# Kernel tuning notes

Hardware: AMD Instinct MI355X
Metric: run time of the kernel (lower is better)

## Reference

```python
import jax, jax.numpy as jnp
import numpy as np

N_NODES = 50000
N_EDGES = 800000
IN_DIM = 256
HIDDEN = 32
HEADS = 4
OUT_DIM = 64


def setup_inputs() -> dict:
    key = jax.random.key(0)
    k1, k2, k3, k4, k5, k6, k7 = jax.random.split(key, 7)
    h = jax.random.normal(k1, (N_NODES, IN_DIM), dtype=jnp.float32)
    src = jax.random.randint(k2, (N_EDGES,), 0, N_NODES, dtype=jnp.int32)
    dst = jax.random.randint(k3, (N_EDGES,), 0, N_NODES, dtype=jnp.int32)
    # xavier_normal with relu gain, per-head weights
    gain = float(np.sqrt(2.0))
    W1 = gain * jnp.sqrt(2.0 / (IN_DIM + HIDDEN)) * jax.random.normal(k4, (HEADS, IN_DIM, HIDDEN), dtype=jnp.float32)
    a1 = gain * jnp.sqrt(2.0 / (2 * HIDDEN + 1)) * jax.random.normal(k5, (HEADS, 2 * HIDDEN), dtype=jnp.float32)
    W2 = gain * jnp.sqrt(2.0 / (HIDDEN * HEADS + OUT_DIM)) * jax.random.normal(k6, (1, HIDDEN * HEADS, OUT_DIM), dtype=jnp.float32)
    a2 = gain * jnp.sqrt(2.0 / (2 * OUT_DIM + 1)) * jax.random.normal(k7, (1, 2 * OUT_DIM), dtype=jnp.float32)
    return {"h": h, "src": src, "dst": dst, "W1": W1, "a1": a1, "W2": W2, "a2": a2}


def _gat_layer(x, src, dst, W, a):
    # x: [N, in], W: [H, in, d], a: [H, 2d]
    N = x.shape[0]
    d = W.shape[-1]
    z = jnp.einsum('ni,hio->nho', x, W)                    # [N, H, d]
    a_s, a_d = a[:, :d], a[:, d:]
    es = jnp.einsum('nho,ho->nh', z, a_s)                  # per-node src score
    ed = jnp.einsum('nho,ho->nh', z, a_d)                  # per-node dst score
    e = jax.nn.leaky_relu(es[src] + ed[dst])               # [E, H]
    # segment (per-destination) softmax over incoming edges
    emax = jax.ops.segment_max(e, dst, num_segments=N)     # [N, H]
    ex = jnp.exp(e - emax[dst])
    denom = jax.ops.segment_sum(ex, dst, num_segments=N)   # [N, H]
    alpha = ex / denom[dst]                                # [E, H]
    # scatter weighted sum of source feats back to destinations
    out = jax.ops.segment_sum(alpha[:, :, None] * z[src], dst, num_segments=N)  # [N, H, d]
    return out.reshape(N, -1)


def reference(h, src, dst, W1, a1, W2, a2):
    h1 = jax.nn.elu(_gat_layer(h, src, dst, W1, a1))       # [N, HEADS*HIDDEN]
    return _gat_layer(h1, src, dst, W2, a2)                # [N, OUT_DIM]
```

## Files before the change

### kernel.cpp

```cpp
#include <hip/hip_runtime.h>
#include <hip/hip_bf16.h>
#include <math.h>

#define N_NODES 50000
#define N_EDGES 800000
#define IN_DIM 256
#define HID 32
#define HEADS 4
#define OUT_DIM 64

#define SCAN_CHUNK 1024
#define SCAN_BLOCKS ((N_NODES + SCAN_CHUNK - 1) / SCAN_CHUNK)

typedef __attribute__((ext_vector_type(8))) short bf16x8;
typedef __attribute__((ext_vector_type(4))) float f32x4;

__device__ __forceinline__ float lrelu(float e) { return e > 0.f ? e : 0.01f * e; }
__device__ __forceinline__ float bflo(unsigned u) { return __uint_as_float(u << 16); }
__device__ __forceinline__ float bfhi(unsigned u) { return __uint_as_float(u & 0xffff0000u); }

__device__ __forceinline__ unsigned short rne_bf16(float x) {
    unsigned u = __float_as_uint(x);
    unsigned r = u + 0x7fffu + ((u >> 16) & 1u);
    return (unsigned short)(r >> 16);
}

__device__ __forceinline__ void splitf(float x, short& hi, short& lo) {
    unsigned u = __float_as_uint(x);
    unsigned short h = (unsigned short)(u >> 16);
    float hf = __uint_as_float(((unsigned)h) << 16);
    float l = x - hf;
    unsigned short lb = (unsigned short)(__float_as_uint(l) >> 16);
    hi = (short)h;
    lo = (short)lb;
}


__global__ void __launch_bounds__(256) prep_kernel(
        const float* __restrict__ W1, const float* __restrict__ a1,
        const float* __restrict__ W2, const float* __restrict__ a2,
        unsigned short* __restrict__ B1h, unsigned short* __restrict__ B1l,
        unsigned short* __restrict__ B2h, unsigned short* __restrict__ B2l,
        int* __restrict__ count) {
    int gid = blockIdx.x * 256 + threadIdx.x;
    if (gid < N_NODES) count[gid] = 0;

    int k = blockIdx.x;
    int c = threadIdx.x;
    if (c < 144) {
        float val = 0.f;
        if (c < 128) {
            val = W1[(size_t)(c >> 5) * IN_DIM * HID + (size_t)k * HID + (c & 31)];
        } else if (c < 136) {
            int j = c - 128;
            int hd = (j < 4) ? j : (j - 4);
            int off = (j < 4) ? 0 : HID;
            const float* Wp = W1 + (size_t)hd * IN_DIM * HID + (size_t)k * HID;
            const float* ap = a1 + hd * 2 * HID + off;
            float s = 0.f;
            for (int o = 0; o < HID; o++) s += Wp[o] * ap[o];
            val = s;
        }
        unsigned short hi = rne_bf16(val);
        float hf = __uint_as_float(((unsigned)hi) << 16);
        unsigned short lo = rne_bf16(val - hf);
        int s_ = k >> 5, q = (k >> 3) & 3, j8 = k & 7;
        int nt = c >> 4, L = q * 16 + (c & 15);
        size_t idx = (((size_t)s_ * 9 + nt) * 64 + L) * 8 + j8;
        B1h[idx] = hi;
        B1l[idx] = lo;
    } else if (c >= 160 && c < 240 && k < 128) {
        int c2 = c - 160;
        float val = 0.f;
        if (c2 < 64) {
            val = W2[(size_t)k * OUT_DIM + c2];
        } else if (c2 < 66) {
            const float* ap = a2 + (c2 - 64) * OUT_DIM;
            const float* Wp = W2 + (size_t)k * OUT_DIM;
            float s = 0.f;
            for (int o = 0; o < OUT_DIM; o++) s += Wp[o] * ap[o];
            val = s;
        }
        unsigned short hi = rne_bf16(val);
        float hf = __uint_as_float(((unsigned)hi) << 16);
        unsigned short lo = rne_bf16(val - hf);
        int s_ = k >> 5, q = (k >> 3) & 3, j8 = k & 7;
        int nt = c2 >> 4, L = q * 16 + (c2 & 15);
        size_t idx = (((size_t)s_ * 5 + nt) * 64 + L) * 8 + j8;
        B2h[idx] = hi;
        B2l[idx] = lo;
    }
}


__global__ void hist_kernel(const int* __restrict__ dst, int* __restrict__ count,
                            int* __restrict__ rank) {
    int i = blockIdx.x * blockDim.x + threadIdx.x;
    if (i < N_EDGES) rank[i] = atomicAdd(&count[dst[i]], 1);
}

__global__ void scan1_kernel(const int* __restrict__ count, int* __restrict__ row_start,
                             int* __restrict__ blocksum) {
    __shared__ int sdata[256];
    int t = threadIdx.x;
    int base = blockIdx.x * SCAN_CHUNK + t * 4;
    int v[4];
    int s = 0;
#pragma unroll
    for (int j = 0; j < 4; j++) {
        int idx = base + j;
        int x = (idx < N_NODES) ? count[idx] : 0;
        v[j] = x;
        s += x;
    }
    sdata[t] = s;
    __syncthreads();
    for (int off = 1; off < 256; off <<= 1) {
        int u = (t >= off) ? sdata[t - off] : 0;
        __syncthreads();
        sdata[t] += u;
        __syncthreads();
    }
    int excl = sdata[t] - s;
#pragma unroll
    for (int j = 0; j < 4; j++) {
        int idx = base + j;
        if (idx < N_NODES) row_start[idx] = excl;
        excl += v[j];
    }
    if (t == 255) blocksum[blockIdx.x] = sdata[255];
}

__global__ void scan23_kernel(int* __restrict__ row_start, const int* __restrict__ blocksum) {
    __shared__ int pre;
    int t = threadIdx.x;
    if (t < 64) {
        int v = (t < SCAN_BLOCKS) ? blocksum[t] : 0;
#pragma unroll
        for (int off = 1; off < 64; off <<= 1) {
            int u = __shfl_up(v, off);
            if (t >= off) v += u;
        }
        if (t == blockIdx.x) pre = v - blocksum[t];
    }
    __syncthreads();
    int add = pre;
    int base = blockIdx.x * SCAN_CHUNK + t * 4;
#pragma unroll
    for (int j = 0; j < 4; j++) {
        int idx = base + j;
        if (idx < N_NODES) row_start[idx] += add;
    }
}

__global__ void scatter_kernel(const int* __restrict__ src, const int* __restrict__ dst,
                               const int* __restrict__ rank, const int* __restrict__ row_start,
                               int* __restrict__ esrc) {
    int i = blockIdx.x * blockDim.x + threadIdx.x;
    if (i < N_EDGES) esrc[row_start[dst[i]] + rank[i]] = src[i];
}


__global__ void __launch_bounds__(256) proj1_mfma(
        const float* __restrict__ h, const unsigned short* __restrict__ Bh,
        const unsigned short* __restrict__ Bl, __hip_bfloat16* __restrict__ z1b,
        float* __restrict__ es1, float* __restrict__ ed1) {
    int tid = threadIdx.x;
    int wave = tid >> 6;
    int L = tid & 63;
    int q = L >> 4, L15 = L & 15;
    int n0 = blockIdx.x * 64 + wave * 16;

    int rowA = n0 + L15;
    int rrA = rowA < N_NODES ? rowA : N_NODES - 1;
    const float* hrow = h + (size_t)rrA * IN_DIM + q * 8;

    f32x4 acc[9];
#pragma unroll
    for (int nt = 0; nt < 9; nt++) acc[nt] = (f32x4)(0.f);

    float4 x0 = *(const float4*)(hrow);
    float4 x1 = *(const float4*)(hrow + 4);

#pragma unroll
    for (int s = 0; s < 8; s++) {
        int sn = (s < 7) ? s + 1 : 7;
        float4 p0 = *(const float4*)(hrow + sn * 32);
        float4 p1 = *(const float4*)(hrow + sn * 32 + 4);

        float xs[8] = {x0.x, x0.y, x0.z, x0.w, x1.x, x1.y, x1.z, x1.w};
        bf16x8 ah, al;
#pragma unroll
        for (int j = 0; j < 8; j++) {
            short hi, lo;
            splitf(xs[j], hi, lo);
            ah[j] = hi;
            al[j] = lo;
        }

        const bf16x8* bhp = (const bf16x8*)(Bh + ((size_t)s * 9 * 64) * 8 + (size_t)L * 8);
        const bf16x8* blp = (const bf16x8*)(Bl + ((size_t)s * 9 * 64) * 8 + (size_t)L * 8);
#pragma unroll
        for (int nt = 0; nt < 9; nt++) {
            bf16x8 bh = bhp[nt * 64];
            acc[nt] = __builtin_amdgcn_mfma_f32_16x16x32_bf16(ah, bh, acc[nt], 0, 0, 0);
            acc[nt] = __builtin_amdgcn_mfma_f32_16x16x32_bf16(al, bh, acc[nt], 0, 0, 0);
        }
        {
            bf16x8 bl8 = blp[8 * 64];
            acc[8] = __builtin_amdgcn_mfma_f32_16x16x32_bf16(ah, bl8, acc[8], 0, 0, 0);
        }
        x0 = p0;
        x1 = p1;
    }

#pragma unroll
    for (int r = 0; r < 4; r++) {
        int rowc = n0 + q * 4 + r;
        if (rowc < N_NODES) {
#pragma unroll
            for (int nt = 0; nt < 8; nt++)
                z1b[(size_t)rowc * 128 + nt * 16 + L15] = __float2bfloat16(acc[nt][r]);
            if (L15 < 4) es1[rowc * HEADS + L15] = acc[8][r];
            else if (L15 < 8) ed1[rowc * HEADS + (L15 - 4)] = acc[8][r];
        }
    }
}


__global__ void __launch_bounds__(256) proj2_mfma(
        const float* __restrict__ h1, const unsigned short* __restrict__ Bh,
        const unsigned short* __restrict__ Bl, __hip_bfloat16* __restrict__ z2b,
        float* __restrict__ es2, float* __restrict__ ed2) {
    int tid = threadIdx.x;
    int wave = tid >> 6;
    int L = tid & 63;
    int q = L >> 4, L15 = L & 15;
    int n0 = blockIdx.x * 64 + wave * 16;

    int rowA = n0 + L15;
    int rrA = rowA < N_NODES ? rowA : N_NODES - 1;
    const float* hrow = h1 + (size_t)rrA * 128 + q * 8;

    f32x4 acc[5];
#pragma unroll
    for (int nt = 0; nt < 5; nt++) acc[nt] = (f32x4)(0.f);

    float4 x0 = *(const float4*)(hrow);
    float4 x1 = *(const float4*)(hrow + 4);

#pragma unroll
    for (int s = 0; s < 4; s++) {
        int sn = (s < 3) ? s + 1 : 3;
        float4 p0 = *(const float4*)(hrow + sn * 32);
        float4 p1 = *(const float4*)(hrow + sn * 32 + 4);

        float xs[8] = {x0.x, x0.y, x0.z, x0.w, x1.x, x1.y, x1.z, x1.w};
        bf16x8 ah, al;
#pragma unroll
        for (int j = 0; j < 8; j++) {
            short hi, lo;
            splitf(xs[j], hi, lo);
            ah[j] = hi;
            al[j] = lo;
        }

        const bf16x8* bhp = (const bf16x8*)(Bh + ((size_t)s * 5 * 64) * 8 + (size_t)L * 8);
        const bf16x8* blp = (const bf16x8*)(Bl + ((size_t)s * 5 * 64) * 8 + (size_t)L * 8);
#pragma unroll
        for (int nt = 0; nt < 5; nt++) {
            bf16x8 bh = bhp[nt * 64];
            acc[nt] = __builtin_amdgcn_mfma_f32_16x16x32_bf16(ah, bh, acc[nt], 0, 0, 0);
            acc[nt] = __builtin_amdgcn_mfma_f32_16x16x32_bf16(al, bh, acc[nt], 0, 0, 0);
        }
        {
            bf16x8 bl4 = blp[4 * 64];
            acc[4] = __builtin_amdgcn_mfma_f32_16x16x32_bf16(ah, bl4, acc[4], 0, 0, 0);
        }
        x0 = p0;
        x1 = p1;
    }

#pragma unroll
    for (int r = 0; r < 4; r++) {
        int rowc = n0 + q * 4 + r;
        if (rowc < N_NODES) {
#pragma unroll
            for (int nt = 0; nt < 4; nt++)
                z2b[(size_t)rowc * OUT_DIM + nt * 16 + L15] = __float2bfloat16(acc[nt][r]);
            if (L15 == 0) es2[rowc] = acc[4][r];
            else if (L15 == 1) ed2[rowc] = acc[4][r];
        }
    }
}


__global__ void __launch_bounds__(256) agg1_kernel(
        const __hip_bfloat16* __restrict__ z1b, const float* __restrict__ es1,
        const float* __restrict__ ed1, const int* __restrict__ row_start,
        const int* __restrict__ count, const int* __restrict__ esrc,
        float* __restrict__ h1) {
    int v = blockIdx.x * 4 + (threadIdx.x >> 6);
    int L = threadIdx.x & 63;
    int half = L >> 5;
    int lj = L & 31;
    int sub = L >> 4;
    int c16 = L & 15;
    int hd = c16 >> 2;
    int srcl = (hd >> 1) << 5;
    int par = hd & 1;
    int beg = row_start[v], deg = count[v];
    float2 edp = *(const float2*)(ed1 + v * 4 + 2 * half);
    float lx = 0.f, ly = 0.f;
    float acc[8];
#pragma unroll
    for (int i = 0; i < 8; i++) acc[i] = 0.f;
    const uint4* zq = (const uint4*)z1b;

    for (int j0 = 0; j0 < deg; j0 += 32) {
        int chunk = min(32, deg - j0);
        bool valid = (j0 + lj) < deg;
        int s_o = 0;
        if (L < 32 && valid) s_o = esrc[beg + j0 + L];
        int s_e = __shfl(s_o, lj);
        float px = 0.f, py = 0.f;
        if (valid) {
            float2 es = *(const float2*)(es1 + (size_t)s_e * 4 + 2 * half);
            px = __expf(lrelu(es.x + edp.x));
            py = __expf(lrelu(es.y + edp.y));
        }
        lx += px;
        ly += py;

        int iters = (chunk + 15) & ~15;
        for (int j = 0; j < iters; j += 16) {
            int se[4];
            float qv[4];
            uint4 u[4];
#pragma unroll
            for (int g = 0; g < 4; g++) {
                int e = j + g * 4 + sub;
                se[g] = __shfl(s_o, e);
                float pxv = __shfl(px, srcl | e);
                float pyv = __shfl(py, srcl | e);
                qv[g] = par ? pyv : pxv;
                u[g] = zq[(size_t)se[g] * 16 + c16];
            }
#pragma unroll
            for (int g = 0; g < 4; g++) {
                acc[0] = fmaf(qv[g], bflo(u[g].x), acc[0]);
                acc[1] = fmaf(qv[g], bfhi(u[g].x), acc[1]);
                acc[2] = fmaf(qv[g], bflo(u[g].y), acc[2]);
                acc[3] = fmaf(qv[g], bfhi(u[g].y), acc[3]);
                acc[4] = fmaf(qv[g], bflo(u[g].z), acc[4]);
                acc[5] = fmaf(qv[g], bfhi(u[g].z), acc[5]);
                acc[6] = fmaf(qv[g], bflo(u[g].w), acc[6]);
                acc[7] = fmaf(qv[g], bfhi(u[g].w), acc[7]);
            }
        }
    }
#pragma unroll
    for (int off = 16; off >= 1; off >>= 1) {
        lx += __shfl_xor(lx, off);
        ly += __shfl_xor(ly, off);
    }
#pragma unroll
    for (int i = 0; i < 8; i++) {
        acc[i] += __shfl_xor(acc[i], 16);
        acc[i] += __shfl_xor(acc[i], 32);
    }
    float lxv = __shfl(lx, srcl);
    float lyv = __shfl(ly, srcl);
    float lmine = par ? lyv : lxv;
    if (L < 16) {
        float4 r0, r1;
#pragma unroll
        for (int i = 0; i < 8; i++) {
            float r = (deg > 0) ? acc[i] / lmine : 0.f;
            r = r > 0.f ? r : expm1f(r);
            if (i < 4) (&r0.x)[i] = r;
            else (&r1.x)[i - 4] = r;
        }
        float* dst = h1 + (size_t)v * 128 + c16 * 8;
        *(float4*)dst = r0;
        *(float4*)(dst + 4) = r1;
    }
}


__global__ void __launch_bounds__(256) agg2_kernel(
        const __hip_bfloat16* __restrict__ z2b, const float* __restrict__ es2,
        const float* __restrict__ ed2, const int* __restrict__ row_start,
        const int* __restrict__ count, const int* __restrict__ esrc,
        float* __restrict__ out) {
    int v = blockIdx.x * 4 + (threadIdx.x >> 6);
    int L = threadIdx.x & 63;
    int sub = L >> 3;
    int c8 = L & 7;
    int beg = row_start[v], deg = count[v];
    float edv = ed2[v];
    float l = 0.f;
    float acc[8];
#pragma unroll
    for (int i = 0; i < 8; i++) acc[i] = 0.f;
    const uint4* zq = (const uint4*)z2b;

    for (int j0 = 0; j0 < deg; j0 += 64) {
        int chunk = min(64, deg - j0);
        int s_o = 0;
        float p_o = 0.f;
        if (j0 + L < deg) {
            s_o = esrc[beg + j0 + L];
            p_o = __expf(lrelu(es2[s_o] + edv));
        }
        l += p_o;

        int iters = (chunk + 15) & ~15;
        for (int j = 0; j < iters; j += 16) {
            int se[2];
            float qv[2];
            uint4 u[2];
#pragma unroll
            for (int g = 0; g < 2; g++) {
                int e = j + g * 8 + sub;
                se[g] = __shfl(s_o, e);
                qv[g] = __shfl(p_o, e);
                u[g] = zq[(size_t)se[g] * 8 + c8];
            }
#pragma unroll
            for (int g = 0; g < 2; g++) {
                acc[0] = fmaf(qv[g], bflo(u[g].x), acc[0]);
                acc[1] = fmaf(qv[g], bfhi(u[g].x), acc[1]);
                acc[2] = fmaf(qv[g], bflo(u[g].y), acc[2]);
                acc[3] = fmaf(qv[g], bfhi(u[g].y), acc[3]);
                acc[4] = fmaf(qv[g], bflo(u[g].z), acc[4]);
                acc[5] = fmaf(qv[g], bfhi(u[g].z), acc[5]);
                acc[6] = fmaf(qv[g], bflo(u[g].w), acc[6]);
                acc[7] = fmaf(qv[g], bfhi(u[g].w), acc[7]);
            }
        }
    }
#pragma unroll
    for (int off = 32; off >= 1; off >>= 1)
        l += __shfl_xor(l, off);
#pragma unroll
    for (int i = 0; i < 8; i++) {
        acc[i] += __shfl_xor(acc[i], 8);
        acc[i] += __shfl_xor(acc[i], 16);
        acc[i] += __shfl_xor(acc[i], 32);
    }
    if (L < 8) {
        float4 r0, r1;
#pragma unroll
        for (int i = 0; i < 8; i++) {
            float r = (deg > 0) ? acc[i] / l : 0.f;
            if (i < 4) (&r0.x)[i] = r;
            else (&r1.x)[i - 4] = r;
        }
        float* dst = out + (size_t)v * OUT_DIM + c8 * 8;
        *(float4*)dst = r0;
        *(float4*)(dst + 4) = r1;
    }
}


extern "C" void kernel_launch(void* const* d_in, const int* in_sizes, int n_in,
                              void* d_out, int out_size, void* d_ws, size_t ws_size,
                              hipStream_t stream) {
    const float* h  = (const float*)d_in[0];
    const int* src  = (const int*)d_in[1];
    const int* dst  = (const int*)d_in[2];
    const float* W1 = (const float*)d_in[3];
    const float* a1 = (const float*)d_in[4];
    const float* W2 = (const float*)d_in[5];
    const float* a2 = (const float*)d_in[6];
    float* out = (float*)d_out;

    char* w = (char*)d_ws;
    size_t off = 0;
    auto alloc = [&](size_t bytes) {
        void* p = w + off;
        off = (off + bytes + 255) & ~(size_t)255;
        return p;
    };
    __hip_bfloat16* z1b = (__hip_bfloat16*)alloc((size_t)N_NODES * 128 * 2);
    float* es1 = (float*)alloc((size_t)N_NODES * HEADS * 4);
    float* ed1 = (float*)alloc((size_t)N_NODES * HEADS * 4);
    float* h1  = (float*)alloc((size_t)N_NODES * 128 * 4);
    __hip_bfloat16* z2b = (__hip_bfloat16*)alloc((size_t)N_NODES * OUT_DIM * 2);
    float* es2 = (float*)alloc((size_t)N_NODES * 4);
    float* ed2 = (float*)alloc((size_t)N_NODES * 4);
    int* count     = (int*)alloc((size_t)N_NODES * 4);
    int* row_start = (int*)alloc((size_t)N_NODES * 4);
    int* rank      = (int*)alloc((size_t)N_EDGES * 4);
    int* blocksum  = (int*)alloc((size_t)SCAN_BLOCKS * 4);
    int* esrc      = (int*)alloc((size_t)N_EDGES * 4);
    unsigned short* Bf1h = (unsigned short*)alloc((size_t)8 * 9 * 64 * 8 * 2);
    unsigned short* Bf1l = (unsigned short*)alloc((size_t)8 * 9 * 64 * 8 * 2);
    unsigned short* Bf2h = (unsigned short*)alloc((size_t)4 * 5 * 64 * 8 * 2);
    unsigned short* Bf2l = (unsigned short*)alloc((size_t)4 * 5 * 64 * 8 * 2);

    prep_kernel<<<256, 256, 0, stream>>>(W1, a1, W2, a2, Bf1h, Bf1l, Bf2h, Bf2l, count);
    hist_kernel<<<(N_EDGES + 255) / 256, 256, 0, stream>>>(dst, count, rank);
    scan1_kernel<<<SCAN_BLOCKS, 256, 0, stream>>>(count, row_start, blocksum);
    scan23_kernel<<<SCAN_BLOCKS, 256, 0, stream>>>(row_start, blocksum);
    scatter_kernel<<<(N_EDGES + 255) / 256, 256, 0, stream>>>(src, dst, rank, row_start, esrc);

    const int MBLK = (N_NODES + 63) / 64;
    proj1_mfma<<<MBLK, 256, 0, stream>>>(h, Bf1h, Bf1l, z1b, es1, ed1);
    agg1_kernel<<<N_NODES / 4, 256, 0, stream>>>(z1b, es1, ed1, row_start, count, esrc, h1);
    proj2_mfma<<<MBLK, 256, 0, stream>>>(h1, Bf2h, Bf2l, z2b, es2, ed2);
    agg2_kernel<<<N_NODES / 4, 256, 0, stream>>>(z2b, es2, ed2, row_start, count, esrc, out);
}
```

Measured before the change: 251.1 us.

## Precompute edge softmax weights in separate kernels and store h1 as bf16

Adds edge1_p and edge2_p kernels that compute exp(leaky_relu) attention numerators per edge in CSR order, so the aggregation kernels no longer gather es scores and compute exps inline. The aggregation loops are restructured to batch 8 (or 4) edge loads before the feature gathers, which exposes more memory-level parallelism. Layer-1 output h1 is now written as bf16 after ELU, and proj2 consumes it directly with a single MFMA pass instead of the hi/lo split. This halves the h1 traffic and MFMA count at the cost of precision, and adds two extra launches plus p1/p2/edst buffers.

```diff
diff --git a/kernel.cpp b/kernel.cpp
--- a/kernel.cpp
+++ b/kernel.cpp
@@ -155,9 +155,14 @@
 
 __global__ void scatter_kernel(const int* __restrict__ src, const int* __restrict__ dst,
                                const int* __restrict__ rank, const int* __restrict__ row_start,
-                               int* __restrict__ esrc) {
+                               int* __restrict__ esrc, int* __restrict__ edst) {
     int i = blockIdx.x * blockDim.x + threadIdx.x;
-    if (i < N_EDGES) esrc[row_start[dst[i]] + rank[i]] = src[i];
+    if (i < N_EDGES) {
+        int d = dst[i];
+        int pos = row_start[d] + rank[i];
+        esrc[pos] = src[i];
+        edst[pos] = d;
+    }
 }
 
 
@@ -228,8 +233,109 @@
 }
 
 
+__global__ void edge1_p(const int* __restrict__ esrc, const int* __restrict__ edst,
+                        const float* __restrict__ es1, const float* __restrict__ ed1,
+                        float* __restrict__ p1) {
+    int pos = blockIdx.x * 256 + threadIdx.x;
+    if (pos >= N_EDGES) return;
+    int s = esrc[pos], d = edst[pos];
+    float4 es = *(const float4*)(es1 + 4 * (size_t)s);
+    float4 ed = *(const float4*)(ed1 + 4 * (size_t)d);
+    p1[0 * (size_t)N_EDGES + pos] = __expf(lrelu(es.x + ed.x));
+    p1[1 * (size_t)N_EDGES + pos] = __expf(lrelu(es.y + ed.y));
+    p1[2 * (size_t)N_EDGES + pos] = __expf(lrelu(es.z + ed.z));
+    p1[3 * (size_t)N_EDGES + pos] = __expf(lrelu(es.w + ed.w));
+}
+
+__global__ void edge2_p(const int* __restrict__ esrc, const int* __restrict__ edst,
+                        const float* __restrict__ es2, const float* __restrict__ ed2,
+                        float* __restrict__ p2) {
+    int pos = blockIdx.x * 256 + threadIdx.x;
+    if (pos >= N_EDGES) return;
+    p2[pos] = __expf(lrelu(es2[esrc[pos]] + ed2[edst[pos]]));
+}
+
+
+__global__ void __launch_bounds__(256) agg1_kernel(
+        const __hip_bfloat16* __restrict__ z1b, const float* __restrict__ p1,
+        const int* __restrict__ row_start, const int* __restrict__ count,
+        const int* __restrict__ esrc, __hip_bfloat16* __restrict__ h1b) {
+    int v = blockIdx.x * 4 + (threadIdx.x >> 6);
+    int L = threadIdx.x & 63;
+    int sub = L >> 4;
+    int c16 = L & 15;
+    int hd = c16 >> 2;
+    int beg = row_start[v], deg = count[v];
+    const float* ph = p1 + (size_t)hd * N_EDGES + beg;
+    const int* ep = esrc + beg;
+    float lacc = 0.f;
+    float acc[8];
+#pragma unroll
+    for (int i = 0; i < 8; i++) acc[i] = 0.f;
+    const uint4* zq = (const uint4*)z1b;
+
+    for (int j0 = 0; j0 < deg; j0 += 32) {
+        int se[8];
+        float q[8];
+        uint4 u[8];
+#pragma unroll
+        for (int g = 0; g < 8; g++) {
+            if (j0 + g * 4 < deg) {
+                int e = j0 + g * 4 + sub;
+                bool val = e < deg;
+                int idx = val ? e : 0;
+                se[g] = ep[idx];
+                float qq = ph[idx];
+                q[g] = val ? qq : 0.f;
+            }
+        }
+#pragma unroll
+        for (int g = 0; g < 8; g++)
+            if (j0 + g * 4 < deg) u[g] = zq[(size_t)se[g] * 16 + c16];
+#pragma unroll
+        for (int g = 0; g < 8; g++) {
+            if (j0 + g * 4 < deg) {
+                lacc += q[g];
+                acc[0] = fmaf(q[g], bflo(u[g].x), acc[0]);
+                acc[1] = fmaf(q[g], bfhi(u[g].x), acc[1]);
+                acc[2] = fmaf(q[g], bflo(u[g].y), acc[2]);
+                acc[3] = fmaf(q[g], bfhi(u[g].y), acc[3]);
+                acc[4] = fmaf(q[g], bflo(u[g].z), acc[4]);
+                acc[5] = fmaf(q[g], bfhi(u[g].z), acc[5]);
+                acc[6] = fmaf(q[g], bflo(u[g].w), acc[6]);
+                acc[7] = fmaf(q[g], bfhi(u[g].w), acc[7]);
+            }
+        }
+    }
+    lacc += __shfl_xor(lacc, 1);
+    lacc += __shfl_xor(lacc, 2);
+    lacc += __shfl_xor(lacc, 16);
+    lacc += __shfl_xor(lacc, 32);
+    lacc *= 0.25f;
+#pragma unroll
+    for (int i = 0; i < 8; i++) {
+        acc[i] += __shfl_xor(acc[i], 16);
+        acc[i] += __shfl_xor(acc[i], 32);
+    }
+    if (L < 16) {
+        float inv = (deg > 0) ? 1.f / lacc : 0.f;
+        unsigned w[4];
+#pragma unroll
+        for (int i = 0; i < 4; i++) {
+            float r0 = acc[2 * i] * inv;
+            float r1 = acc[2 * i + 1] * inv;
+            r0 = r0 > 0.f ? r0 : __expf(r0) - 1.f;
+            r1 = r1 > 0.f ? r1 : __expf(r1) - 1.f;
+            w[i] = (unsigned)rne_bf16(r0) | ((unsigned)rne_bf16(r1) << 16);
+        }
+        uint4* dst = (uint4*)(h1b + (size_t)v * 128 + c16 * 8);
+        *dst = make_uint4(w[0], w[1], w[2], w[3]);
+    }
+}
+
+
 __global__ void __launch_bounds__(256) proj2_mfma(
-        const float* __restrict__ h1, const unsigned short* __restrict__ Bh,
+        const __hip_bfloat16* __restrict__ h1b, const unsigned short* __restrict__ Bh,
         const unsigned short* __restrict__ Bl, __hip_bfloat16* __restrict__ z2b,
         float* __restrict__ es2, float* __restrict__ ed2) {
     int tid = threadIdx.x;
@@ -240,45 +346,21 @@
 
     int rowA = n0 + L15;
     int rrA = rowA < N_NODES ? rowA : N_NODES - 1;
-    const float* hrow = h1 + (size_t)rrA * 128 + q * 8;
+    const bf16x8* hq = (const bf16x8*)(h1b + (size_t)rrA * 128);
 
     f32x4 acc[5];
 #pragma unroll
     for (int nt = 0; nt < 5; nt++) acc[nt] = (f32x4)(0.f);
 
-    float4 x0 = *(const float4*)(hrow);
-    float4 x1 = *(const float4*)(hrow + 4);
-
 #pragma unroll
     for (int s = 0; s < 4; s++) {
-        int sn = (s < 3) ? s + 1 : 3;
-        float4 p0 = *(const float4*)(hrow + sn * 32);
-        float4 p1 = *(const float4*)(hrow + sn * 32 + 4);
-
-        float xs[8] = {x0.x, x0.y, x0.z, x0.w, x1.x, x1.y, x1.z, x1.w};
-        bf16x8 ah, al;
-#pragma unroll
-        for (int j = 0; j < 8; j++) {
-            short hi, lo;
-            splitf(xs[j], hi, lo);
-            ah[j] = hi;
-            al[j] = lo;
-        }
-
+        bf16x8 a = hq[s * 4 + q];
         const bf16x8* bhp = (const bf16x8*)(Bh + ((size_t)s * 5 * 64) * 8 + (size_t)L * 8);
         const bf16x8* blp = (const bf16x8*)(Bl + ((size_t)s * 5 * 64) * 8 + (size_t)L * 8);
 #pragma unroll
-        for (int nt = 0; nt < 5; nt++) {
-            bf16x8 bh = bhp[nt * 64];
-            acc[nt] = __builtin_amdgcn_mfma_f32_16x16x32_bf16(ah, bh, acc[nt], 0, 0, 0);
-            acc[nt] = __builtin_amdgcn_mfma_f32_16x16x32_bf16(al, bh, acc[nt], 0, 0, 0);
-        }
-        {
-            bf16x8 bl4 = blp[4 * 64];
-            acc[4] = __builtin_amdgcn_mfma_f32_16x16x32_bf16(ah, bl4, acc[4], 0, 0, 0);
-        }
-        x0 = p0;
-        x1 = p1;
+        for (int nt = 0; nt < 5; nt++)
+            acc[nt] = __builtin_amdgcn_mfma_f32_16x16x32_bf16(a, bhp[nt * 64], acc[nt], 0, 0, 0);
+        acc[4] = __builtin_amdgcn_mfma_f32_16x16x32_bf16(a, blp[4 * 64], acc[4], 0, 0, 0);
     }
 
 #pragma unroll
@@ -295,154 +377,59 @@
 }
 
 
-__global__ void __launch_bounds__(256) agg1_kernel(
-        const __hip_bfloat16* __restrict__ z1b, const float* __restrict__ es1,
-        const float* __restrict__ ed1, const int* __restrict__ row_start,
-        const int* __restrict__ count, const int* __restrict__ esrc,
-        float* __restrict__ h1) {
-    int v = blockIdx.x * 4 + (threadIdx.x >> 6);
-    int L = threadIdx.x & 63;
-    int half = L >> 5;
-    int lj = L & 31;
-    int sub = L >> 4;
-    int c16 = L & 15;
-    int hd = c16 >> 2;
-    int srcl = (hd >> 1) << 5;
-    int par = hd & 1;
-    int beg = row_start[v], deg = count[v];
-    float2 edp = *(const float2*)(ed1 + v * 4 + 2 * half);
-    float lx = 0.f, ly = 0.f;
-    float acc[8];
-#pragma unroll
-    for (int i = 0; i < 8; i++) acc[i] = 0.f;
-    const uint4* zq = (const uint4*)z1b;
-
-    for (int j0 = 0; j0 < deg; j0 += 32) {
-        int chunk = min(32, deg - j0);
-        bool valid = (j0 + lj) < deg;
-        int s_o = 0;
-        if (L < 32 && valid) s_o = esrc[beg + j0 + L];
-        int s_e = __shfl(s_o, lj);
-        float px = 0.f, py = 0.f;
-        if (valid) {
-            float2 es = *(const float2*)(es1 + (size_t)s_e * 4 + 2 * half);
-            px = __expf(lrelu(es.x + edp.x));
-            py = __expf(lrelu(es.y + edp.y));
-        }
-        lx += px;
-        ly += py;
-
-        int iters = (chunk + 15) & ~15;
-        for (int j = 0; j < iters; j += 16) {
-            int se[4];
-            float qv[4];
-            uint4 u[4];
-#pragma unroll
-            for (int g = 0; g < 4; g++) {
-                int e = j + g * 4 + sub;
-                se[g] = __shfl(s_o, e);
-                float pxv = __shfl(px, srcl | e);
-                float pyv = __shfl(py, srcl | e);
-                qv[g] = par ? pyv : pxv;
-                u[g] = zq[(size_t)se[g] * 16 + c16];
-            }
-#pragma unroll
-            for (int g = 0; g < 4; g++) {
-                acc[0] = fmaf(qv[g], bflo(u[g].x), acc[0]);
-                acc[1] = fmaf(qv[g], bfhi(u[g].x), acc[1]);
-                acc[2] = fmaf(qv[g], bflo(u[g].y), acc[2]);
-                acc[3] = fmaf(qv[g], bfhi(u[g].y), acc[3]);
-                acc[4] = fmaf(qv[g], bflo(u[g].z), acc[4]);
-                acc[5] = fmaf(qv[g], bfhi(u[g].z), acc[5]);
-                acc[6] = fmaf(qv[g], bflo(u[g].w), acc[6]);
-                acc[7] = fmaf(qv[g], bfhi(u[g].w), acc[7]);
-            }
-        }
-    }
-#pragma unroll
-    for (int off = 16; off >= 1; off >>= 1) {
-        lx += __shfl_xor(lx, off);
-        ly += __shfl_xor(ly, off);
-    }
-#pragma unroll
-    for (int i = 0; i < 8; i++) {
-        acc[i] += __shfl_xor(acc[i], 16);
-        acc[i] += __shfl_xor(acc[i], 32);
-    }
-    float lxv = __shfl(lx, srcl);
-    float lyv = __shfl(ly, srcl);
-    float lmine = par ? lyv : lxv;
-    if (L < 16) {
-        float4 r0, r1;
-#pragma unroll
-        for (int i = 0; i < 8; i++) {
-            float r = (deg > 0) ? acc[i] / lmine : 0.f;
-            r = r > 0.f ? r : expm1f(r);
-            if (i < 4) (&r0.x)[i] = r;
-            else (&r1.x)[i - 4] = r;
-        }
-        float* dst = h1 + (size_t)v * 128 + c16 * 8;
-        *(float4*)dst = r0;
-        *(float4*)(dst + 4) = r1;
-    }
-}
-
-
 __global__ void __launch_bounds__(256) agg2_kernel(
-        const __hip_bfloat16* __restrict__ z2b, const float* __restrict__ es2,
-        const float* __restrict__ ed2, const int* __restrict__ row_start,
-        const int* __restrict__ count, const int* __restrict__ esrc,
-        float* __restrict__ out) {
+        const __hip_bfloat16* __restrict__ z2b, const float* __restrict__ p2,
+        const int* __restrict__ row_start, const int* __restrict__ count,
+        const int* __restrict__ esrc, float* __restrict__ out) {
     int v = blockIdx.x * 4 + (threadIdx.x >> 6);
     int L = threadIdx.x & 63;
     int sub = L >> 3;
     int c8 = L & 7;
     int beg = row_start[v], deg = count[v];
-    float edv = ed2[v];
-    float l = 0.f;
+    const float* ph = p2 + beg;
+    const int* ep = esrc + beg;
+    float lacc = 0.f;
     float acc[8];
 #pragma unroll
     for (int i = 0; i < 8; i++) acc[i] = 0.f;
     const uint4* zq = (const uint4*)z2b;
 
-    for (int j0 = 0; j0 < deg; j0 += 64) {
-        int chunk = min(64, deg - j0);
-        int s_o = 0;
-        float p_o = 0.f;
-        if (j0 + L < deg) {
-            s_o = esrc[beg + j0 + L];
-            p_o = __expf(lrelu(es2[s_o] + edv));
-        }
-        l += p_o;
-
-        int iters = (chunk + 15) & ~15;
-        for (int j = 0; j < iters; j += 16) {
-            int se[2];
-            float qv[2];
-            uint4 u[2];
-#pragma unroll
-            for (int g = 0; g < 2; g++) {
-                int e = j + g * 8 + sub;
-                se[g] = __shfl(s_o, e);
-                qv[g] = __shfl(p_o, e);
-                u[g] = zq[(size_t)se[g] * 8 + c8];
+    for (int j0 = 0; j0 < deg; j0 += 32) {
+        int se[4];
+        float q[4];
+        uint4 u[4];
+#pragma unroll
+        for (int g = 0; g < 4; g++) {
+            if (j0 + g * 8 < deg) {
+                int e = j0 + g * 8 + sub;
+                bool val = e < deg;
+                int idx = val ? e : 0;
+                se[g] = ep[idx];
+                float qq = ph[idx];
+                q[g] = val ? qq : 0.f;
             }
-#pragma unroll
-            for (int g = 0; g < 2; g++) {
-                acc[0] = fmaf(qv[g], bflo(u[g].x), acc[0]);
-                acc[1] = fmaf(qv[g], bfhi(u[g].x), acc[1]);
-                acc[2] = fmaf(qv[g], bflo(u[g].y), acc[2]);
-                acc[3] = fmaf(qv[g], bfhi(u[g].y), acc[3]);
-                acc[4] = fmaf(qv[g], bflo(u[g].z), acc[4]);
-                acc[5] = fmaf(qv[g], bfhi(u[g].z), acc[5]);
-                acc[6] = fmaf(qv[g], bflo(u[g].w), acc[6]);
-                acc[7] = fmaf(qv[g], bfhi(u[g].w), acc[7]);
+        }
+#pragma unroll
+        for (int g = 0; g < 4; g++)
+            if (j0 + g * 8 < deg) u[g] = zq[(size_t)se[g] * 8 + c8];
+#pragma unroll
+        for (int g = 0; g < 4; g++) {
+            if (j0 + g * 8 < deg) {
+                lacc += q[g];
+                acc[0] = fmaf(q[g], bflo(u[g].x), acc[0]);
+                acc[1] = fmaf(q[g], bfhi(u[g].x), acc[1]);
+                acc[2] = fmaf(q[g], bflo(u[g].y), acc[2]);
+                acc[3] = fmaf(q[g], bfhi(u[g].y), acc[3]);
+                acc[4] = fmaf(q[g], bflo(u[g].z), acc[4]);
+                acc[5] = fmaf(q[g], bfhi(u[g].z), acc[5]);
+                acc[6] = fmaf(q[g], bflo(u[g].w), acc[6]);
+                acc[7] = fmaf(q[g], bfhi(u[g].w), acc[7]);
             }
         }
     }
-#pragma unroll
-    for (int off = 32; off >= 1; off >>= 1)
-        l += __shfl_xor(l, off);
+    lacc += __shfl_xor(lacc, 8);
+    lacc += __shfl_xor(lacc, 16);
+    lacc += __shfl_xor(lacc, 32);
 #pragma unroll
     for (int i = 0; i < 8; i++) {
         acc[i] += __shfl_xor(acc[i], 8);
@@ -450,10 +437,11 @@
         acc[i] += __shfl_xor(acc[i], 32);
     }
     if (L < 8) {
+        float inv = (deg > 0) ? 1.f / lacc : 0.f;
         float4 r0, r1;
 #pragma unroll
         for (int i = 0; i < 8; i++) {
-            float r = (deg > 0) ? acc[i] / l : 0.f;
+            float r = acc[i] * inv;
             if (i < 4) (&r0.x)[i] = r;
             else (&r1.x)[i - 4] = r;
         }
@@ -486,7 +474,7 @@
     __hip_bfloat16* z1b = (__hip_bfloat16*)alloc((size_t)N_NODES * 128 * 2);
     float* es1 = (float*)alloc((size_t)N_NODES * HEADS * 4);
     float* ed1 = (float*)alloc((size_t)N_NODES * HEADS * 4);
-    float* h1  = (float*)alloc((size_t)N_NODES * 128 * 4);
+    __hip_bfloat16* h1b = (__hip_bfloat16*)alloc((size_t)N_NODES * 128 * 2);
     __hip_bfloat16* z2b = (__hip_bfloat16*)alloc((size_t)N_NODES * OUT_DIM * 2);
     float* es2 = (float*)alloc((size_t)N_NODES * 4);
     float* ed2 = (float*)alloc((size_t)N_NODES * 4);
@@ -495,6 +483,9 @@
     int* rank      = (int*)alloc((size_t)N_EDGES * 4);
     int* blocksum  = (int*)alloc((size_t)SCAN_BLOCKS * 4);
     int* esrc      = (int*)alloc((size_t)N_EDGES * 4);
+    int* edst      = (int*)alloc((size_t)N_EDGES * 4);
+    float* p1      = (float*)alloc((size_t)N_EDGES * HEADS * 4);
+    float* p2      = (float*)alloc((size_t)N_EDGES * 4);
     unsigned short* Bf1h = (unsigned short*)alloc((size_t)8 * 9 * 64 * 8 * 2);
     unsigned short* Bf1l = (unsigned short*)alloc((size_t)8 * 9 * 64 * 8 * 2);
     unsigned short* Bf2h = (unsigned short*)alloc((size_t)4 * 5 * 64 * 8 * 2);
@@ -504,11 +495,13 @@
     hist_kernel<<<(N_EDGES + 255) / 256, 256, 0, stream>>>(dst, count, rank);
     scan1_kernel<<<SCAN_BLOCKS, 256, 0, stream>>>(count, row_start, blocksum);
     scan23_kernel<<<SCAN_BLOCKS, 256, 0, stream>>>(row_start, blocksum);
-    scatter_kernel<<<(N_EDGES + 255) / 256, 256, 0, stream>>>(src, dst, rank, row_start, esrc);
+    scatter_kernel<<<(N_EDGES + 255) / 256, 256, 0, stream>>>(src, dst, rank, row_start, esrc, edst);
 
     const int MBLK = (N_NODES + 63) / 64;
     proj1_mfma<<<MBLK, 256, 0, stream>>>(h, Bf1h, Bf1l, z1b, es1, ed1);
-    agg1_kernel<<<N_NODES / 4, 256, 0, stream>>>(z1b, es1, ed1, row_start, count, esrc, h1);
-    proj2_mfma<<<MBLK, 256, 0, stream>>>(h1, Bf2h, Bf2l, z2b, es2, ed2);
-    agg2_kernel<<<N_NODES / 4, 256, 0, stream>>>(z2b, es2, ed2, row_start, count, esrc, out);
-}
+    edge1_p<<<(N_EDGES + 255) / 256, 256, 0, stream>>>(esrc, edst, es1, ed1, p1);
+    agg1_kernel<<<N_NODES / 4, 256, 0, stream>>>(z1b, p1, row_start, count, esrc, h1b);
+    proj2_mfma<<<MBLK, 256, 0, stream>>>(h1b, Bf2h, Bf2l, z2b, es2, ed2);
+    edge2_p<<<(N_EDGES + 255) / 256, 256, 0, stream>>>(esrc, edst, es2, ed2, p2);
+    agg2_kernel<<<N_NODES / 4, 256, 0, stream>>>(z2b, p2, row_start, count, esrc, out);
+}
```

New measurement: 268.3 us. 1.07x slower.
